# Kernel optimization log

Measured on AMD Instinct MI355X. Metric: run time of the kernel, lower is better.

Reference implementation:

```python
import jax, jax.numpy as jnp
import numpy as np

SOFTCAP = 30.0

def setup_inputs() -> dict:
    key = jax.random.key(0)
    ks = jax.random.split(key, 5)
    T, D, F, E = 8192, 2048, 4096, 8
    s_in = 1.0 / np.sqrt(D)
    s_mid = 1.0 / np.sqrt(F)
    return {
        "hidden_states": jax.random.normal(ks[0], (T, D), jnp.float32),
        "gate_w": jax.random.normal(ks[1], (D, E), jnp.float32) * s_in,
        "w_gate": jax.random.normal(ks[2], (E, D, F), jnp.float32) * s_in,
        "w_up": jax.random.normal(ks[3], (E, D, F), jnp.float32) * s_in,
        "w_down": jax.random.normal(ks[4], (E, F, D), jnp.float32) * s_mid,
        "top_k": 2,
    }

def reference(hidden_states, gate_w, w_gate, w_up, w_down, top_k):
    x = hidden_states
    T = x.shape[0]
    # --- router: fp32 gate, tanh softcap, softmax ---
    logits = x.astype(jnp.float32) @ gate_w                      # [T, E]
    logits = jnp.tanh(logits / SOFTCAP) * SOFTCAP
    probs = jax.nn.softmax(logits, axis=-1)                      # [T, E]
    # --- top-k selection (weights are the softmax probs, no renorm) ---
    weights, idx = jax.lax.top_k(probs, top_k)                   # [T, k]
    combine = jnp.zeros_like(probs).at[jnp.arange(T)[:, None], idx].set(
        weights.astype(probs.dtype))                              # [T, E]
    combine = combine.astype(x.dtype)
    # --- expert MLPs: gelu(x@w_gate) * (x@w_up) @ w_down, scan over E ---
    def step(acc, ewts):
        wg, wu, wd, c = ewts                                     # [D,F],[D,F],[F,D],[T]
        h = jax.nn.gelu(x @ wg) * (x @ wu)                       # [T, F]
        return acc + c[:, None] * (h @ wd), None
    out, _ = jax.lax.scan(step, jnp.zeros_like(x),
                          (w_gate, w_up, w_down, combine.T))
    return out
```

## Files before the change

### kernel.cpp

```cpp
#include <hip/hip_runtime.h>
#include <hip/hip_bf16.h>
#include <cstdint>
#include <cstddef>

#define TNUM 8192
#define DDIM 2048
#define FDIM 4096
#define NEXP 8

typedef __attribute__((ext_vector_type(4))) float f32x4;
typedef __attribute__((ext_vector_type(4))) unsigned u32x4;
typedef __attribute__((ext_vector_type(8))) short s16x8;
typedef __attribute__((ext_vector_type(8))) __bf16 bf16x8v;

__device__ inline f32x4 mfma16(s16x8 a, s16x8 b, f32x4 c) {
  return __builtin_amdgcn_mfma_f32_16x16x32_bf16(
      __builtin_bit_cast(bf16x8v, a), __builtin_bit_cast(bf16x8v, b), c, 0, 0, 0);
}

__device__ inline unsigned short bf16r(float f) {
  union { float f; unsigned u; } x; x.f = f;
  unsigned r = x.u + 0x7fffu + ((x.u >> 16) & 1u);
  return (unsigned short)(r >> 16);
}

__device__ inline unsigned pk2(float a, float b) {
  __hip_bfloat162 h = __float22bfloat162_rn(make_float2(a, b));
  unsigned r;
  __builtin_memcpy(&r, &h, 4);
  return r;
}

__device__ inline int swz16(int row, int b) {
  return (row << 7) + (b ^ ((row & 7) << 4));
}

typedef const __attribute__((address_space(1))) void* gp_t;
typedef __attribute__((address_space(3))) void* lp_t;
__device__ inline void gl16(const void* g, void* l) {
  __builtin_amdgcn_global_load_lds((gp_t)g, (lp_t)l, 16, 0, 0);
}

#define FENCE asm volatile("" ::: "memory")

__global__ __launch_bounds__(256) void k_router(
    const float* __restrict__ x, const float* __restrict__ gw,
    int* __restrict__ top_idx, float* __restrict__ top_w, int* __restrict__ counts) {
  __shared__ float gwT[NEXP][DDIM];
  const int tid = threadIdx.x;
  for (int i = tid; i < NEXP * DDIM; i += 256) {
    int d = i >> 3, e = i & 7;
    gwT[e][d] = gw[i];
  }
  __syncthreads();
  const int lane = tid & 63;
  const int t = blockIdx.x * 4 + (tid >> 6);
  const float4* xr = (const float4*)(x + (size_t)t * DDIM);
  double acc[NEXP];
#pragma unroll
  for (int e = 0; e < NEXP; e++) acc[e] = 0.0;
  for (int d4 = lane; d4 < DDIM / 4; d4 += 64) {
    float4 xv = xr[d4];
#pragma unroll
    for (int e = 0; e < NEXP; e++) {
      float4 gv = *(const float4*)&gwT[e][d4 * 4];
      acc[e] += (double)xv.x * gv.x + (double)xv.y * gv.y +
                (double)xv.z * gv.z + (double)xv.w * gv.w;
    }
  }
#pragma unroll
  for (int e = 0; e < NEXP; e++) {
    double v = acc[e];
#pragma unroll
    for (int s = 32; s > 0; s >>= 1) v += __shfl_xor(v, s);
    acc[e] = v;
  }
  if (lane == 0) {
    int i0 = 0; double b0 = acc[0];
#pragma unroll
    for (int e = 1; e < NEXP; e++) if (acc[e] > b0) { b0 = acc[e]; i0 = e; }
    int i1 = (i0 == 0) ? 1 : 0; double b1 = acc[i1];
#pragma unroll
    for (int e = 0; e < NEXP; e++) {
      if (e == i0 || e == i1) continue;
      if (acc[e] > b1) { b1 = acc[e]; i1 = e; }
    }
    float lc[NEXP]; float mx = -1e30f;
#pragma unroll
    for (int e = 0; e < NEXP; e++) {
      lc[e] = tanhf((float)(acc[e] * (1.0 / 30.0))) * 30.0f;
      mx = lc[e] > mx ? lc[e] : mx;
    }
    float s = 0.0f;
#pragma unroll
    for (int e = 0; e < NEXP; e++) { lc[e] = expf(lc[e] - mx); s += lc[e]; }
    float inv = 1.0f / s;
    top_idx[t * 2] = i0; top_idx[t * 2 + 1] = i1;
    top_w[t * 2] = lc[i0] * inv; top_w[t * 2 + 1] = lc[i1] * inv;
    atomicAdd(&counts[i0], 1);
    atomicAdd(&counts[i1], 1);
  }
}

__global__ void k_scan(const int* __restrict__ counts, int* __restrict__ offs,
                       int* __restrict__ cursor) {
  if (threadIdx.x == 0) {
    int s = 0;
    for (int e = 0; e < NEXP; e++) { offs[e] = s; cursor[e] = s; s += counts[e]; }
    offs[NEXP] = s;
  }
}

__global__ void k_scatter(const int* __restrict__ top_idx, const float* __restrict__ top_w,
                          int* __restrict__ cursor, int* __restrict__ perm_tok,
                          float* __restrict__ perm_w) {
  int t = blockIdx.x * 256 + threadIdx.x;
#pragma unroll
  for (int k = 0; k < 2; k++) {
    int e = top_idx[t * 2 + k];
    int pos = atomicAdd(&cursor[e], 1);
    perm_tok[pos] = t;
    perm_w[pos] = top_w[t * 2 + k];
  }
}

__global__ void k_cast(const float* __restrict__ x, unsigned short* __restrict__ xb) {
  size_t i = ((size_t)blockIdx.x * 256 + threadIdx.x) * 8;
  f32x4 a = *(const f32x4*)(x + i);
  f32x4 b = *(const f32x4*)(x + i + 4);
  u32x4 v;
  v[0] = pk2(a[0], a[1]); v[1] = pk2(a[2], a[3]);
  v[2] = pk2(b[0], b[1]); v[3] = pk2(b[2], b[3]);
  *(u32x4*)(xb + i) = v;
}

__global__ __launch_bounds__(256) void k_convT(
    const float* __restrict__ src, unsigned short* __restrict__ dst,
    int K, int N, int cmap) {
  __shared__ char ct[8192];
  const int e = blockIdx.z;
  const float* src_e = src + (size_t)e * K * N;
  const int nout = cmap ? 2 * N : N;
  unsigned short* dst_e = dst + (size_t)e * nout * K;
  const int k0 = blockIdx.y * 64, n0 = blockIdx.x * 64;
  const int tid = threadIdx.x;
#pragma unroll
  for (int i = 0; i < 4; i++) {
    int idx = tid + i * 256;
    int kr = idx >> 4, f4 = idx & 15;
    f32x4 v = *(const f32x4*)(src_e + (size_t)(k0 + kr) * N + n0 + f4 * 4);
#pragma unroll
    for (int j = 0; j < 4; j++) {
      int n = f4 * 4 + j;
      *(unsigned short*)(ct + n * 128 + ((kr * 2) ^ ((n & 7) << 4))) = bf16r(v[j]);
    }
  }
  __syncthreads();
#pragma unroll
  for (int i = 0; i < 2; i++) {
    int s = tid + i * 256;
    int n = s >> 3, ks = s & 7;
    int gn = n0 + n;
    int cd = cmap ? (((gn >> 4) << 5) + (gn & 15) + (cmap == 2 ? 16 : 0)) : gn;
    s16x8 val = *(const s16x8*)(ct + n * 128 + ((ks * 16) ^ ((n & 7) << 4)));
    *(s16x8*)(dst_e + (size_t)cd * K + k0 + ks * 8) = val;
  }
}

__global__ __launch_bounds__(256) void k_mlp1(
    const unsigned short* __restrict__ xb, const unsigned short* __restrict__ wguT,
    const int* __restrict__ perm_tok, const int* __restrict__ offs,
    unsigned short* __restrict__ H) {
  __shared__ char lds[65536];
  const int e = blockIdx.z;
  const int off = offs[e], cnt = offs[e + 1] - off;
  const int nb = blockIdx.x * 128;
  const unsigned short* wgu_e = wguT + (size_t)e * 2 * DDIM * FDIM;
  const int tid = threadIdx.x;
  const int lane = tid & 63;
  const int wr = tid >> 7, wc = (tid >> 6) & 1;
  const int l15 = lane & 15, lk = lane >> 4;
  const int wbase = (tid >> 6) * 1024;

#pragma unroll 1
  for (int mt = blockIdx.y; mt * 128 < cnt; mt += 16) {
    const unsigned short* asrc[4];
    const unsigned short* bsrc[4];
#pragma unroll
    for (int i = 0; i < 4; i++) {
      int seg = tid + i * 256;
      int m = seg >> 3, kp = (seg & 7) ^ (m & 7);
      int gm = mt * 128 + m;
      if (gm >= cnt) gm = cnt - 1;
      asrc[i] = xb + (size_t)perm_tok[off + gm] * DDIM + kp * 8;
      bsrc[i] = wgu_e + (size_t)(nb + m) * DDIM + kp * 8;
    }
    f32x4 acc[4][4];
#pragma unroll
    for (int mi = 0; mi < 4; mi++)
#pragma unroll
      for (int ni = 0; ni < 4; ni++) acc[mi][ni] = f32x4{0.f, 0.f, 0.f, 0.f};

#define STAGE1(buf, koff)                                        \
    {                                                            \
      char* As_ = lds + (buf) * 32768;                           \
      char* Bs_ = As_ + 16384;                                   \
      _Pragma("unroll") for (int i = 0; i < 4; i++) {            \
        gl16(asrc[i] + (koff), As_ + i * 4096 + wbase);          \
        gl16(bsrc[i] + (koff), Bs_ + i * 4096 + wbase);          \
      }                                                          \
    }

    STAGE1(0, 0);
    int cur = 0;
#pragma unroll 1
    for (int t = 0; t < DDIM / 64; t++) {
      if (t + 1 < DDIM / 64) {
        STAGE1(cur ^ 1, (t + 1) * 64);
        asm volatile("s_waitcnt vmcnt(8)" ::: "memory");
      } else {
        asm volatile("s_waitcnt vmcnt(0)" ::: "memory");
      }
      FENCE;
      __builtin_amdgcn_s_barrier();
      FENCE;
      {
        char* As_ = lds + cur * 32768;
        char* Bs_ = As_ + 16384;
#pragma unroll
        for (int ks = 0; ks < 2; ks++) {
          s16x8 a[4];
#pragma unroll
          for (int mi = 0; mi < 4; mi++)
            a[mi] = *(const s16x8*)(As_ + swz16(wr * 64 + mi * 16 + l15, ks * 64 + lk * 16));
#pragma unroll
          for (int ni = 0; ni < 4; ni++) {
            s16x8 b = *(const s16x8*)(Bs_ + swz16(wc * 64 + ni * 16 + l15, ks * 64 + lk * 16));
#pragma unroll
            for (int mi = 0; mi < 4; mi++) acc[mi][ni] = mfma16(a[mi], b, acc[mi][ni]);
          }
        }
      }
      FENCE;
      __builtin_amdgcn_s_barrier();
      FENCE;
      cur ^= 1;
    }
#undef STAGE1

#pragma unroll
    for (int mi = 0; mi < 4; mi++) {
      int rb = wr * 64 + mi * 16 + lk * 4;
#pragma unroll
      for (int j = 0; j < 4; j++) {
        int gm = mt * 128 + rb + j;
        if (gm < cnt) {
          unsigned short* hrow = H + (size_t)(off + gm) * FDIM;
#pragma unroll
          for (int ni = 0; ni < 4; ni += 2) {
            int jj = (nb >> 4) + wc * 4 + ni;
            int hc = ((jj >> 1) << 4) + l15;
            float g = acc[mi][ni][j];
            float u = acc[mi][ni + 1][j];
            float x3 = g * g * g;
            float gl = 0.5f * g * (1.0f + tanhf(0.7978845608f * (g + 0.044715f * x3)));
            hrow[hc] = bf16r(gl * u);
          }
        }
      }
    }
  }
}

__global__ __launch_bounds__(256) void k_mlp2(
    const unsigned short* __restrict__ H, const unsigned short* __restrict__ wdT,
    const int* __restrict__ perm_tok, const float* __restrict__ perm_w,
    const int* __restrict__ offs, float* __restrict__ out) {
  __shared__ char lds[65536];
  const int e = blockIdx.z;
  const int off = offs[e], cnt = offs[e + 1] - off;
  const int nb = blockIdx.x * 128;
  const unsigned short* wd_e = wdT + (size_t)e * FDIM * DDIM;
  const int tid = threadIdx.x;
  const int lane = tid & 63;
  const int wr = tid >> 7, wc = (tid >> 6) & 1;
  const int l15 = lane & 15, lk = lane >> 4;
  const int wbase = (tid >> 6) * 1024;

#pragma unroll 1
  for (int mt = blockIdx.y; mt * 128 < cnt; mt += 16) {
    const unsigned short* asrc[4];
    const unsigned short* bsrc[4];
#pragma unroll
    for (int i = 0; i < 4; i++) {
      int seg = tid + i * 256;
      int m = seg >> 3, kp = (seg & 7) ^ (m & 7);
      int gm = mt * 128 + m;
      if (gm >= cnt) gm = cnt - 1;
      asrc[i] = H + (size_t)(off + gm) * FDIM + kp * 8;
      bsrc[i] = wd_e + (size_t)(nb + m) * FDIM + kp * 8;
    }
    f32x4 acc[4][4];
#pragma unroll
    for (int mi = 0; mi < 4; mi++)
#pragma unroll
      for (int ni = 0; ni < 4; ni++) acc[mi][ni] = f32x4{0.f, 0.f, 0.f, 0.f};

#define STAGE2(buf, koff)                                        \
    {                                                            \
      char* As_ = lds + (buf) * 32768;                           \
      char* Bs_ = As_ + 16384;                                   \
      _Pragma("unroll") for (int i = 0; i < 4; i++) {            \
        gl16(asrc[i] + (koff), As_ + i * 4096 + wbase);          \
        gl16(bsrc[i] + (koff), Bs_ + i * 4096 + wbase);          \
      }                                                          \
    }

    STAGE2(0, 0);
    int cur = 0;
#pragma unroll 1
    for (int t = 0; t < FDIM / 64; t++) {
      if (t + 1 < FDIM / 64) {
        STAGE2(cur ^ 1, (t + 1) * 64);
        asm volatile("s_waitcnt vmcnt(8)" ::: "memory");
      } else {
        asm volatile("s_waitcnt vmcnt(0)" ::: "memory");
      }
      FENCE;
      __builtin_amdgcn_s_barrier();
      FENCE;
      {
        char* As_ = lds + cur * 32768;
        char* Bs_ = As_ + 16384;
#pragma unroll
        for (int ks = 0; ks < 2; ks++) {
          s16x8 a[4];
#pragma unroll
          for (int mi = 0; mi < 4; mi++)
            a[mi] = *(const s16x8*)(As_ + swz16(wr * 64 + mi * 16 + l15, ks * 64 + lk * 16));
#pragma unroll
          for (int ni = 0; ni < 4; ni++) {
            s16x8 b = *(const s16x8*)(Bs_ + swz16(wc * 64 + ni * 16 + l15, ks * 64 + lk * 16));
#pragma unroll
            for (int mi = 0; mi < 4; mi++) acc[mi][ni] = mfma16(a[mi], b, acc[mi][ni]);
          }
        }
      }
      FENCE;
      __builtin_amdgcn_s_barrier();
      FENCE;
      cur ^= 1;
    }
#undef STAGE2

#pragma unroll
    for (int mi = 0; mi < 4; mi++) {
      int rb = wr * 64 + mi * 16 + lk * 4;
#pragma unroll
      for (int j = 0; j < 4; j++) {
        int gm = mt * 128 + rb + j;
        if (gm < cnt) {
          int tok = perm_tok[off + gm];
          float w = perm_w[off + gm];
          float* orow = out + (size_t)tok * DDIM + nb + wc * 64 + l15;
#pragma unroll
          for (int ni = 0; ni < 4; ni++) atomicAdd(&orow[ni * 16], w * acc[mi][ni][j]);
        }
      }
    }
  }
}

extern "C" void kernel_launch(void* const* d_in, const int* in_sizes, int n_in,
                              void* d_out, int out_size, void* d_ws, size_t ws_size,
                              hipStream_t stream) {
  const float* x = (const float*)d_in[0];
  const float* gw = (const float*)d_in[1];
  const float* wgate = (const float*)d_in[2];
  const float* wup = (const float*)d_in[3];
  const float* wdown = (const float*)d_in[4];
  float* out = (float*)d_out;

  const size_t XB_B = 33554432;
  const size_t H_B = 134217728;
  const size_t WGU_B = 268435456;
  const size_t WD_B = 134217728;

  char* ws = (char*)d_ws;
  unsigned short* xb = (unsigned short*)ws;
  unsigned short* H = (unsigned short*)(ws + XB_B);
  unsigned short* wguT = (unsigned short*)(ws + XB_B + H_B);
  unsigned short* wdT = (unsigned short*)(ws + XB_B + H_B + WGU_B);
  char* meta = ws + XB_B + H_B + WGU_B + WD_B;
  int* counts = (int*)(meta);
  int* offs = (int*)(meta + 64);
  int* cursor = (int*)(meta + 128);
  int* top_idx = (int*)(meta + 256);
  float* top_w = (float*)(meta + 256 + 65536);
  int* perm_tok = (int*)(meta + 256 + 131072);
  float* perm_w = (float*)(meta + 256 + 196608);

  (void)hipMemsetAsync(counts, 0, 64, stream);
  (void)hipMemsetAsync(d_out, 0, (size_t)TNUM * DDIM * 4, stream);
  k_router<<<TNUM / 4, 256, 0, stream>>>(x, gw, top_idx, top_w, counts);
  k_scan<<<1, 64, 0, stream>>>(counts, offs, cursor);
  k_scatter<<<TNUM / 256, 256, 0, stream>>>(top_idx, top_w, cursor, perm_tok, perm_w);
  k_cast<<<(TNUM * DDIM / 8) / 256, 256, 0, stream>>>(x, xb);
  k_convT<<<dim3(FDIM / 64, DDIM / 64, NEXP), 256, 0, stream>>>(wgate, wguT, DDIM, FDIM, 1);
  k_convT<<<dim3(FDIM / 64, DDIM / 64, NEXP), 256, 0, stream>>>(wup, wguT, DDIM, FDIM, 2);
  k_convT<<<dim3(DDIM / 64, FDIM / 64, NEXP), 256, 0, stream>>>(wdown, wdT, FDIM, DDIM, 0);
  k_mlp1<<<dim3(2 * FDIM / 128, 16, NEXP), 256, 0, stream>>>(xb, wguT, perm_tok, offs, H);
  k_mlp2<<<dim3(DDIM / 128, 16, NEXP), 256, 0, stream>>>(H, wdT, perm_tok, perm_w, offs, out);
}
```

Measured before the change: 1.405 ms.

## Enlarge MoE GEMM tiles to 256x256 with 8 waves and 128KB LDS

Both expert GEMM kernels move from 128x128 tiles with 4 waves to 256x256 tiles with 8 waves, each wave computing a 128x64 sub-tile held in 32 accumulators. Shared memory becomes a dynamic 128KB double buffer. s_setprio wraps the MFMA section. The aim is more reuse per loaded byte and fewer global loads per FLOP. In exchange it raises register pressure, leaves fewer blocks in the grid (which can hurt load balance across uneven expert counts), and with 128KB LDS the launch_bounds occupancy hint of 2 cannot be met, so only one block fits per CU.

```diff
diff --git a/kernel.cpp b/kernel.cpp
--- a/kernel.cpp
+++ b/kernel.cpp
@@ -167,47 +167,48 @@
   }
 }
 
-__global__ __launch_bounds__(256) void k_mlp1(
+__global__ __launch_bounds__(512, 2) void k_mlp1(
     const unsigned short* __restrict__ xb, const unsigned short* __restrict__ wguT,
     const int* __restrict__ perm_tok, const int* __restrict__ offs,
     unsigned short* __restrict__ H) {
-  __shared__ char lds[65536];
+  extern __shared__ char lds[];
   const int e = blockIdx.z;
   const int off = offs[e], cnt = offs[e + 1] - off;
-  const int nb = blockIdx.x * 128;
+  const int nb = blockIdx.x * 256;
   const unsigned short* wgu_e = wguT + (size_t)e * 2 * DDIM * FDIM;
   const int tid = threadIdx.x;
   const int lane = tid & 63;
-  const int wr = tid >> 7, wc = (tid >> 6) & 1;
+  const int wid = tid >> 6;
+  const int wr = wid >> 2, wc = wid & 3;
   const int l15 = lane & 15, lk = lane >> 4;
-  const int wbase = (tid >> 6) * 1024;
+  const int wbase = wid * 1024;
 
 #pragma unroll 1
-  for (int mt = blockIdx.y; mt * 128 < cnt; mt += 16) {
+  for (int mt = blockIdx.y; mt * 256 < cnt; mt += 8) {
     const unsigned short* asrc[4];
     const unsigned short* bsrc[4];
 #pragma unroll
     for (int i = 0; i < 4; i++) {
-      int seg = tid + i * 256;
+      int seg = tid + i * 512;
       int m = seg >> 3, kp = (seg & 7) ^ (m & 7);
-      int gm = mt * 128 + m;
+      int gm = mt * 256 + m;
       if (gm >= cnt) gm = cnt - 1;
       asrc[i] = xb + (size_t)perm_tok[off + gm] * DDIM + kp * 8;
       bsrc[i] = wgu_e + (size_t)(nb + m) * DDIM + kp * 8;
     }
-    f32x4 acc[4][4];
-#pragma unroll
-    for (int mi = 0; mi < 4; mi++)
+    f32x4 acc[8][4];
+#pragma unroll
+    for (int mi = 0; mi < 8; mi++)
 #pragma unroll
       for (int ni = 0; ni < 4; ni++) acc[mi][ni] = f32x4{0.f, 0.f, 0.f, 0.f};
 
 #define STAGE1(buf, koff)                                        \
     {                                                            \
-      char* As_ = lds + (buf) * 32768;                           \
-      char* Bs_ = As_ + 16384;                                   \
+      char* As_ = lds + (buf) * 65536;                           \
+      char* Bs_ = As_ + 32768;                                   \
       _Pragma("unroll") for (int i = 0; i < 4; i++) {            \
-        gl16(asrc[i] + (koff), As_ + i * 4096 + wbase);          \
-        gl16(bsrc[i] + (koff), Bs_ + i * 4096 + wbase);          \
+        gl16(asrc[i] + (koff), As_ + i * 8192 + wbase);          \
+        gl16(bsrc[i] + (koff), Bs_ + i * 8192 + wbase);          \
       }                                                          \
     }
 
@@ -225,21 +226,30 @@
       __builtin_amdgcn_s_barrier();
       FENCE;
       {
-        char* As_ = lds + cur * 32768;
-        char* Bs_ = As_ + 16384;
+        char* As_ = lds + cur * 65536;
+        char* Bs_ = As_ + 32768;
+        __builtin_amdgcn_s_setprio(1);
 #pragma unroll
         for (int ks = 0; ks < 2; ks++) {
-          s16x8 a[4];
-#pragma unroll
-          for (int mi = 0; mi < 4; mi++)
-            a[mi] = *(const s16x8*)(As_ + swz16(wr * 64 + mi * 16 + l15, ks * 64 + lk * 16));
-#pragma unroll
-          for (int ni = 0; ni < 4; ni++) {
-            s16x8 b = *(const s16x8*)(Bs_ + swz16(wc * 64 + ni * 16 + l15, ks * 64 + lk * 16));
-#pragma unroll
-            for (int mi = 0; mi < 4; mi++) acc[mi][ni] = mfma16(a[mi], b, acc[mi][ni]);
+          s16x8 b[4];
+#pragma unroll
+          for (int ni = 0; ni < 4; ni++)
+            b[ni] = *(const s16x8*)(Bs_ + swz16(wc * 64 + ni * 16 + l15, ks * 64 + lk * 16));
+#pragma unroll
+          for (int mih = 0; mih < 2; mih++) {
+            s16x8 a[4];
+#pragma unroll
+            for (int mi = 0; mi < 4; mi++)
+              a[mi] = *(const s16x8*)(As_ + swz16(wr * 128 + mih * 64 + mi * 16 + l15,
+                                                 ks * 64 + lk * 16));
+#pragma unroll
+            for (int ni = 0; ni < 4; ni++)
+#pragma unroll
+              for (int mi = 0; mi < 4; mi++)
+                acc[mih * 4 + mi][ni] = mfma16(a[mi], b[ni], acc[mih * 4 + mi][ni]);
           }
         }
+        __builtin_amdgcn_s_setprio(0);
       }
       FENCE;
       __builtin_amdgcn_s_barrier();
@@ -249,19 +259,19 @@
 #undef STAGE1
 
 #pragma unroll
-    for (int mi = 0; mi < 4; mi++) {
-      int rb = wr * 64 + mi * 16 + lk * 4;
+    for (int am = 0; am < 8; am++) {
+      int rb = wr * 128 + am * 16 + lk * 4;
 #pragma unroll
       for (int j = 0; j < 4; j++) {
-        int gm = mt * 128 + rb + j;
+        int gm = mt * 256 + rb + j;
         if (gm < cnt) {
           unsigned short* hrow = H + (size_t)(off + gm) * FDIM;
 #pragma unroll
           for (int ni = 0; ni < 4; ni += 2) {
             int jj = (nb >> 4) + wc * 4 + ni;
             int hc = ((jj >> 1) << 4) + l15;
-            float g = acc[mi][ni][j];
-            float u = acc[mi][ni + 1][j];
+            float g = acc[am][ni][j];
+            float u = acc[am][ni + 1][j];
             float x3 = g * g * g;
             float gl = 0.5f * g * (1.0f + tanhf(0.7978845608f * (g + 0.044715f * x3)));
             hrow[hc] = bf16r(gl * u);
@@ -272,47 +282,48 @@
   }
 }
 
-__global__ __launch_bounds__(256) void k_mlp2(
+__global__ __launch_bounds__(512, 2) void k_mlp2(
     const unsigned short* __restrict__ H, const unsigned short* __restrict__ wdT,
     const int* __restrict__ perm_tok, const float* __restrict__ perm_w,
     const int* __restrict__ offs, float* __restrict__ out) {
-  __shared__ char lds[65536];
+  extern __shared__ char lds[];
   const int e = blockIdx.z;
   const int off = offs[e], cnt = offs[e + 1] - off;
-  const int nb = blockIdx.x * 128;
+  const int nb = blockIdx.x * 256;
   const unsigned short* wd_e = wdT + (size_t)e * FDIM * DDIM;
   const int tid = threadIdx.x;
   const int lane = tid & 63;
-  const int wr = tid >> 7, wc = (tid >> 6) & 1;
+  const int wid = tid >> 6;
+  const int wr = wid >> 2, wc = wid & 3;
   const int l15 = lane & 15, lk = lane >> 4;
-  const int wbase = (tid >> 6) * 1024;
+  const int wbase = wid * 1024;
 
 #pragma unroll 1
-  for (int mt = blockIdx.y; mt * 128 < cnt; mt += 16) {
+  for (int mt = blockIdx.y; mt * 256 < cnt; mt += 8) {
     const unsigned short* asrc[4];
     const unsigned short* bsrc[4];
 #pragma unroll
     for (int i = 0; i < 4; i++) {
-      int seg = tid + i * 256;
+      int seg = tid + i * 512;
       int m = seg >> 3, kp = (seg & 7) ^ (m & 7);
-      int gm = mt * 128 + m;
+      int gm = mt * 256 + m;
       if (gm >= cnt) gm = cnt - 1;
       asrc[i] = H + (size_t)(off + gm) * FDIM + kp * 8;
       bsrc[i] = wd_e + (size_t)(nb + m) * FDIM + kp * 8;
     }
-    f32x4 acc[4][4];
-#pragma unroll
-    for (int mi = 0; mi < 4; mi++)
+    f32x4 acc[8][4];
+#pragma unroll
+    for (int mi = 0; mi < 8; mi++)
 #pragma unroll
       for (int ni = 0; ni < 4; ni++) acc[mi][ni] = f32x4{0.f, 0.f, 0.f, 0.f};
 
 #define STAGE2(buf, koff)                                        \
     {                                                            \
-      char* As_ = lds + (buf) * 32768;                           \
-      char* Bs_ = As_ + 16384;                                   \
+      char* As_ = lds + (buf) * 65536;                           \
+      char* Bs_ = As_ + 32768;                                   \
       _Pragma("unroll") for (int i = 0; i < 4; i++) {            \
-        gl16(asrc[i] + (koff), As_ + i * 4096 + wbase);          \
-        gl16(bsrc[i] + (koff), Bs_ + i * 4096 + wbase);          \
+        gl16(asrc[i] + (koff), As_ + i * 8192 + wbase);          \
+        gl16(bsrc[i] + (koff), Bs_ + i * 8192 + wbase);          \
       }                                                          \
     }
 
@@ -330,21 +341,30 @@
       __builtin_amdgcn_s_barrier();
       FENCE;
       {
-        char* As_ = lds + cur * 32768;
-        char* Bs_ = As_ + 16384;
+        char* As_ = lds + cur * 65536;
+        char* Bs_ = As_ + 32768;
+        __builtin_amdgcn_s_setprio(1);
 #pragma unroll
         for (int ks = 0; ks < 2; ks++) {
-          s16x8 a[4];
-#pragma unroll
-          for (int mi = 0; mi < 4; mi++)
-            a[mi] = *(const s16x8*)(As_ + swz16(wr * 64 + mi * 16 + l15, ks * 64 + lk * 16));
-#pragma unroll
-          for (int ni = 0; ni < 4; ni++) {
-            s16x8 b = *(const s16x8*)(Bs_ + swz16(wc * 64 + ni * 16 + l15, ks * 64 + lk * 16));
-#pragma unroll
-            for (int mi = 0; mi < 4; mi++) acc[mi][ni] = mfma16(a[mi], b, acc[mi][ni]);
+          s16x8 b[4];
+#pragma unroll
+          for (int ni = 0; ni < 4; ni++)
+            b[ni] = *(const s16x8*)(Bs_ + swz16(wc * 64 + ni * 16 + l15, ks * 64 + lk * 16));
+#pragma unroll
+          for (int mih = 0; mih < 2; mih++) {
+            s16x8 a[4];
+#pragma unroll
+            for (int mi = 0; mi < 4; mi++)
+              a[mi] = *(const s16x8*)(As_ + swz16(wr * 128 + mih * 64 + mi * 16 + l15,
+                                                 ks * 64 + lk * 16));
+#pragma unroll
+            for (int ni = 0; ni < 4; ni++)
+#pragma unroll
+              for (int mi = 0; mi < 4; mi++)
+                acc[mih * 4 + mi][ni] = mfma16(a[mi], b[ni], acc[mih * 4 + mi][ni]);
           }
         }
+        __builtin_amdgcn_s_setprio(0);
       }
       FENCE;
       __builtin_amdgcn_s_barrier();
@@ -354,17 +374,17 @@
 #undef STAGE2
 
 #pragma unroll
-    for (int mi = 0; mi < 4; mi++) {
-      int rb = wr * 64 + mi * 16 + lk * 4;
+    for (int am = 0; am < 8; am++) {
+      int rb = wr * 128 + am * 16 + lk * 4;
 #pragma unroll
       for (int j = 0; j < 4; j++) {
-        int gm = mt * 128 + rb + j;
+        int gm = mt * 256 + rb + j;
         if (gm < cnt) {
           int tok = perm_tok[off + gm];
           float w = perm_w[off + gm];
           float* orow = out + (size_t)tok * DDIM + nb + wc * 64 + l15;
 #pragma unroll
-          for (int ni = 0; ni < 4; ni++) atomicAdd(&orow[ni * 16], w * acc[mi][ni][j]);
+          for (int ni = 0; ni < 4; ni++) atomicAdd(&orow[ni * 16], w * acc[am][ni][j]);
         }
       }
     }
@@ -400,6 +420,11 @@
   int* perm_tok = (int*)(meta + 256 + 131072);
   float* perm_w = (float*)(meta + 256 + 196608);
 
+  (void)hipFuncSetAttribute((const void*)k_mlp1,
+                            hipFuncAttributeMaxDynamicSharedMemorySize, 131072);
+  (void)hipFuncSetAttribute((const void*)k_mlp2,
+                            hipFuncAttributeMaxDynamicSharedMemorySize, 131072);
+
   (void)hipMemsetAsync(counts, 0, 64, stream);
   (void)hipMemsetAsync(d_out, 0, (size_t)TNUM * DDIM * 4, stream);
   k_router<<<TNUM / 4, 256, 0, stream>>>(x, gw, top_idx, top_w, counts);
@@ -409,6 +434,6 @@
   k_convT<<<dim3(FDIM / 64, DDIM / 64, NEXP), 256, 0, stream>>>(wgate, wguT, DDIM, FDIM, 1);
   k_convT<<<dim3(FDIM / 64, DDIM / 64, NEXP), 256, 0, stream>>>(wup, wguT, DDIM, FDIM, 2);
   k_convT<<<dim3(DDIM / 64, FDIM / 64, NEXP), 256, 0, stream>>>(wdown, wdT, FDIM, DDIM, 0);
-  k_mlp1<<<dim3(2 * FDIM / 128, 16, NEXP), 256, 0, stream>>>(xb, wguT, perm_tok, offs, H);
-  k_mlp2<<<dim3(DDIM / 128, 16, NEXP), 256, 0, stream>>>(H, wdT, perm_tok, perm_w, offs, out);
-}
+  k_mlp1<<<dim3(2 * FDIM / 256, 8, NEXP), 512, 131072, stream>>>(xb, wguT, perm_tok, offs, H);
+  k_mlp2<<<dim3(DDIM / 256, 8, NEXP), 512, 131072, stream>>>(H, wdT, perm_tok, perm_w, offs, out);
+}
```

Measured after the change: 1.593 ms. 13.4% more time.
